# Optimization experiments

Measured on AMD Instinct MI355X. Metric: run time of the kernel, lower is better.

## Reference

```python
import jax, jax.numpy as jnp
import numpy as np

B, S, IN, E, H, FF, L = 8, 1024, 128, 512, 8, 2048, 4
HD = E // H
EPS = 1e-5


def make_pe(seq_len, d_model):
    position = np.arange(seq_len, dtype=np.float32)[:, None]
    div_term = np.exp(np.arange(0, d_model, 2, dtype=np.float32) * (-np.log(10000.0) / d_model))
    pe = np.zeros((seq_len, d_model), dtype=np.float32)
    pe[:, 0::2] = np.sin(position * div_term)
    pe[:, 1::2] = np.cos(position * div_term)
    return jnp.asarray(pe)


def setup_inputs() -> dict:
    key = jax.random.key(0)
    ks = jax.random.split(key, 16)
    s = 0.02
    return {
        "src": jax.random.normal(ks[0], (B, S, IN), jnp.float32),
        "distances": jax.random.uniform(ks[1], (B, S, S), jnp.float32),
        "proj_w": jax.random.normal(ks[2], (E, IN), jnp.float32) * s,
        "proj_b": jnp.zeros((E,), jnp.float32),
        "bn_g": jnp.ones((E,), jnp.float32),
        "bn_b": jnp.zeros((E,), jnp.float32),
        "in_proj_w": jax.random.normal(ks[3], (3 * E, E), jnp.float32) * s,
        "in_proj_b": jnp.zeros((3 * E,), jnp.float32),
        "dist_scale": jnp.array(1.0, jnp.float32),
        "lin1_w": jax.random.normal(ks[4], (FF, E), jnp.float32) * s,
        "lin1_b": jnp.zeros((FF,), jnp.float32),
        "lin2_w": jax.random.normal(ks[5], (E, FF), jnp.float32) * s,
        "lin2_b": jnp.zeros((E,), jnp.float32),
        "n1_g": jnp.ones((E,), jnp.float32),
        "n1_b": jnp.zeros((E,), jnp.float32),
        "n2_g": jnp.ones((E,), jnp.float32),
        "n2_b": jnp.zeros((E,), jnp.float32),
    }


def layernorm(x, g, b):
    m = jnp.mean(x, axis=-1, keepdims=True)
    v = jnp.var(x, axis=-1, keepdims=True)
    return (x - m) * jax.lax.rsqrt(v + EPS) * g + b


def reference(src, distances, proj_w, proj_b, bn_g, bn_b, in_proj_w, in_proj_b,
              dist_scale, lin1_w, lin1_b, lin2_w, lin2_b, n1_g, n1_b, n2_g, n2_b):
    # input projection
    x = jnp.einsum('bsi,ei->bse', src, proj_w) + proj_b  # [B,S,E]
    # BatchNorm1d over flattened (B*S) dim, training-mode batch stats
    xf = x.reshape(-1, E)
    mu = jnp.mean(xf, axis=0)
    var = jnp.var(xf, axis=0)
    x = ((xf - mu) * jax.lax.rsqrt(var + EPS) * bn_g + bn_b).reshape(B, S, E)
    # positional encoding
    x = x + make_pe(S, E)[None]
    # distance bias (same for every layer)
    dmax = jnp.max(distances, axis=-1, keepdims=True)
    dist_bias = jnp.exp(dist_scale * (1.0 - distances / dmax))  # [B,S,S]
    scale = 1.0 / jnp.sqrt(jnp.float32(HD))
    # num_layers iterations of the SAME (shared-parameter) layer
    for _ in range(L):
        qkv = jnp.einsum('bse,fe->bsf', x, in_proj_w) + in_proj_b  # [B,S,3E]
        q, k, v = jnp.split(qkv, 3, axis=-1)
        q = q.reshape(B, S, H, HD).transpose(0, 2, 1, 3)
        k = k.reshape(B, S, H, HD).transpose(0, 2, 1, 3)
        scores = jnp.einsum('bhqd,bhkd->bhqk', q, k) * scale  # [B,H,S,S]
        attn = jax.nn.softmax(scores, axis=-1)
        avg_w = jnp.mean(attn, axis=1)  # head-averaged weights [B,S,S]
        w = avg_w * dist_bias
        w = w / jnp.sum(w, axis=-1, keepdims=True)
        # NOTE: original bmm uses raw layer input as value (no V/out projection)
        attn_out = jnp.einsum('bqk,bke->bqe', w, x)
        x = layernorm(x + attn_out, n1_g, n1_b)
        ff = jnp.einsum('bsf,ef->bse', jax.nn.relu(jnp.einsum('bse,fe->bsf', x, lin1_w) + lin1_b), lin2_w) + lin2_b
        x = layernorm(x + ff, n2_g, n2_b)
    return x
```

## Files before the change

kernel.cpp:

```cpp
#include <hip/hip_runtime.h>
#include <hip/hip_bf16.h>
#include <math.h>

#define Bz 8
#define Sz 1024
#define INz 128
#define Ez 512
#define Hz 8
#define HDz 64
#define FFz 2048
#define Lz 4
#define Nz (Bz*Sz)
#define EPSf 1e-5f

typedef __attribute__((ext_vector_type(8))) short short8;
typedef __attribute__((ext_vector_type(4))) float floatx4;
#define MFMA16(a,b,c) __builtin_amdgcn_mfma_f32_16x16x32_bf16(a,b,c,0,0,0)

typedef __hip_bfloat16 bf16;

__device__ inline float b2f(bf16 v) { return __bfloat162float(v); }
__device__ inline bf16 f2b(float v) { return __float2bfloat16(v); }

__device__ inline void gload16(const bf16* g, bf16* lds_base)
{
  __builtin_amdgcn_global_load_lds(
      (const __attribute__((address_space(1))) void*)g,
      (__attribute__((address_space(3))) void*)lds_base,
      16, 0, 0);
}

#define FENCE() asm volatile("" ::: "memory")
#define PB() do { FENCE(); __builtin_amdgcn_s_barrier(); FENCE(); } while (0)
#define VMCNT0() asm volatile("s_waitcnt vmcnt(0)" ::: "memory")
#define VMCNT8() asm volatile("s_waitcnt vmcnt(8)" ::: "memory")

__global__ __launch_bounds__(256) void cast_f2b(const float* __restrict__ in,
    bf16* __restrict__ out, int n)
{
  int i = blockIdx.x * 256 + threadIdx.x;
  if (i < n) out[i] = f2b(in[i]);
}

__global__ __launch_bounds__(512, 1) void gemm256(
    const bf16* __restrict__ A, const bf16* __restrict__ Wm,
    const float* __restrict__ bias, bf16* __restrict__ Cb,
    int N, int K, int relu)
{
  int gx = gridDim.x, nwg = gx * gridDim.y;
  int flat = blockIdx.y * gx + blockIdx.x;
  if (!(nwg & 7)) {
    int cpx = nwg >> 3;
    flat = (flat & 7) * cpx + (flat >> 3);
  }
  int bm = (flat / gx) * 256, bn = (flat % gx) * 256;
  __shared__ __align__(16) bf16 As0[256][64], Bs0[256][64];
  __shared__ __align__(16) bf16 As1[256][64], Bs1[256][64];
  int t = threadIdx.x, wave = t >> 6, lane = t & 63;
  int wm = (wave >> 2) * 128, wn = (wave & 3) * 64;
  int fr = lane & 15, fo = lane >> 4;
  int w8 = wave * 8, lrow = lane >> 3;
  int sc8 = ((lane & 7) ^ (lrow & 7)) * 8;
  floatx4 acc[8][4];
  #pragma unroll
  for (int i = 0; i < 8; ++i)
    #pragma unroll
    for (int j = 0; j < 4; ++j) acc[i][j] = (floatx4){0.f, 0.f, 0.f, 0.f};

  #define STAGE8(DA, DB, kk) do {                                           \
    _Pragma("unroll")                                                        \
    for (int c_ = 0; c_ < 4; ++c_) {                                         \
      int row_ = c_ * 64 + w8 + lrow;                                        \
      gload16(A  + (size_t)(bm + row_) * K + (kk) + sc8, &DA[c_ * 64 + w8][0]);\
      gload16(Wm + (size_t)(bn + row_) * K + (kk) + sc8, &DB[c_ * 64 + w8][0]);\
    } } while (0)

  #define TILE(AA, BB, SA, SB, kk, DOSTAGE) do {                            \
    _Pragma("unroll")                                                        \
    for (int q_ = 0; q_ < 4; ++q_) {                                         \
      short8 a_[4][2], bf_[2][2];                                            \
      _Pragma("unroll")                                                      \
      for (int j_ = 0; j_ < 4; ++j_) {                                       \
        int row_ = wm + ((q_ >> 1) * 4 + j_) * 16 + fr;                      \
        a_[j_][0] = *(const short8*)&AA[row_][((fo) ^ (fr & 7)) * 8];        \
        a_[j_][1] = *(const short8*)&AA[row_][((4 + fo) ^ (fr & 7)) * 8];    \
      }                                                                      \
      _Pragma("unroll")                                                      \
      for (int g_ = 0; g_ < 2; ++g_) {                                       \
        int row_ = wn + ((q_ & 1) * 2 + g_) * 16 + fr;                       \
        bf_[g_][0] = *(const short8*)&BB[row_][((fo) ^ (fr & 7)) * 8];       \
        bf_[g_][1] = *(const short8*)&BB[row_][((4 + fo) ^ (fr & 7)) * 8];   \
      }                                                                      \
      if ((DOSTAGE) && q_ == 0) STAGE8(SA, SB, kk);                          \
      PB();                                                                  \
      __builtin_amdgcn_s_setprio(1);                                         \
      _Pragma("unroll")                                                      \
      for (int j_ = 0; j_ < 4; ++j_)                                         \
        _Pragma("unroll")                                                    \
        for (int g_ = 0; g_ < 2; ++g_) {                                     \
          int fi_ = (q_ >> 1) * 4 + j_, gi_ = (q_ & 1) * 2 + g_;             \
          acc[fi_][gi_] = MFMA16(a_[j_][0], bf_[g_][0], acc[fi_][gi_]);      \
          acc[fi_][gi_] = MFMA16(a_[j_][1], bf_[g_][1], acc[fi_][gi_]);      \
        }                                                                    \
      __builtin_amdgcn_s_setprio(0);                                         \
      if (q_ == 3) VMCNT0();                                                 \
      PB();                                                                  \
    } } while (0)

  int nt = K >> 6;
  STAGE8(As0, Bs0, 0);
  STAGE8(As1, Bs1, 64);
  VMCNT8();
  PB();
  TILE(As0, Bs0, As0, Bs0, 0, 0);
  for (int i = 1; i + 2 < nt; i += 2) {
    TILE(As1, Bs1, As0, Bs0, (i + 1) * 64, 1);
    TILE(As0, Bs0, As1, Bs1, (i + 2) * 64, 1);
  }
  TILE(As1, Bs1, As0, Bs0, 0, 0);
  #undef STAGE8
  #undef TILE

  #pragma unroll
  for (int f = 0; f < 8; ++f) {
    #pragma unroll
    for (int r = 0; r < 4; ++r) {
      int row = bm + wm + f * 16 + (lane >> 4) * 4 + r;
      #pragma unroll
      for (int g = 0; g < 4; ++g) {
        int col = bn + wn + g * 16 + fr;
        float v = acc[f][g][r] + (bias ? bias[col] : 0.f);
        if (relu) v = fmaxf(v, 0.f);
        Cb[(size_t)row * N + col] = f2b(v);
      }
    }
  }
}

__global__ __launch_bounds__(256) void gemm_bt(
    const bf16* __restrict__ A, const bf16* __restrict__ Wm,
    const float* __restrict__ bias, float* __restrict__ Cf,
    bf16* __restrict__ Cb, const float* __restrict__ rowscale,
    int M, int N, int K, long sA, long sW, long sC, int relu)
{
  int z = blockIdx.z;
  A  += (size_t)z * sA;
  Wm += (size_t)z * sW;
  if (rowscale) rowscale += (size_t)z * M;
  size_t cbase = (size_t)z * sC;
  int bm = blockIdx.y * 128, bn = blockIdx.x * 128;
  __shared__ __align__(16) bf16 As0[128][64], Bs0[128][64];
  __shared__ __align__(16) bf16 As1[128][64], Bs1[128][64];
  int t = threadIdx.x, wave = t >> 6, lane = t & 63;
  int wm = (wave >> 1) * 64, wn = (wave & 1) * 64;
  int fr = lane & 15, fo = lane >> 4;
  int srow = lane >> 3;
  int scol = ((lane & 7) ^ srow) * 8;
  floatx4 acc[4][4];
  #pragma unroll
  for (int i = 0; i < 4; ++i)
    #pragma unroll
    for (int j = 0; j < 4; ++j) acc[i][j] = (floatx4){0.f, 0.f, 0.f, 0.f};

  #define STAGE(Ad, Bd, kk) do {                                            \
    _Pragma("unroll")                                                        \
    for (int i_ = 0; i_ < 4; ++i_) {                                         \
      int chunk_ = wave * 4 + i_;                                            \
      int row_ = chunk_ * 8 + srow;                                          \
      gload16(A  + (size_t)(bm + row_) * K + (kk) + scol, &Ad[chunk_ * 8][0]);\
      gload16(Wm + (size_t)(bn + row_) * K + (kk) + scol, &Bd[chunk_ * 8][0]);\
    } } while (0)

  #define COMPUTE(Ad, Bd) do {                                               \
    _Pragma("unroll")                                                        \
    for (int ks_ = 0; ks_ < 2; ++ks_) {                                      \
      int sw_ = ((ks_ * 4 + fo) ^ (fr & 7)) * 8;                             \
      short8 af_[4], bf_[4];                                                 \
      _Pragma("unroll")                                                      \
      for (int rt_ = 0; rt_ < 4; ++rt_)                                      \
        af_[rt_] = *(const short8*)&Ad[wm + rt_ * 16 + fr][sw_];             \
      _Pragma("unroll")                                                      \
      for (int ct_ = 0; ct_ < 4; ++ct_)                                      \
        bf_[ct_] = *(const short8*)&Bd[wn + ct_ * 16 + fr][sw_];             \
      _Pragma("unroll")                                                      \
      for (int rt_ = 0; rt_ < 4; ++rt_)                                      \
        _Pragma("unroll")                                                    \
        for (int ct_ = 0; ct_ < 4; ++ct_)                                    \
          acc[rt_][ct_] = MFMA16(af_[rt_], bf_[ct_], acc[rt_][ct_]);         \
    } } while (0)

  STAGE(As0, Bs0, 0);
  __syncthreads();
  for (int k0 = 0; k0 < K; k0 += 128) {
    if (k0 + 64 < K) STAGE(As1, Bs1, k0 + 64);
    COMPUTE(As0, Bs0);
    __syncthreads();
    if (k0 + 64 < K) {
      if (k0 + 128 < K) STAGE(As0, Bs0, k0 + 128);
      COMPUTE(As1, Bs1);
      __syncthreads();
    }
  }
  #undef STAGE
  #undef COMPUTE

  #pragma unroll
  for (int rt = 0; rt < 4; ++rt) {
    #pragma unroll
    for (int r = 0; r < 4; ++r) {
      int row = bm + wm + rt * 16 + (lane >> 4) * 4 + r;
      float rs = rowscale ? (1.f / rowscale[row]) : 1.f;
      #pragma unroll
      for (int ct = 0; ct < 4; ++ct) {
        int col = bn + wn + ct * 16 + fr;
        float v = acc[rt][ct][r] + (bias ? bias[col] : 0.f);
        if (relu) v = fmaxf(v, 0.f);
        v *= rs;
        if (Cf) Cf[cbase + (size_t)row * N + col] = v;
        if (Cb) Cb[cbase + (size_t)row * N + col] = f2b(v);
      }
    }
  }
}

__global__ __launch_bounds__(256) void bn_stats(const float* __restrict__ x, float* __restrict__ st)
{
  int c = blockIdx.x;
  float s = 0.f, q = 0.f;
  for (int r = threadIdx.x; r < Nz; r += 256) {
    float v = x[(size_t)r * Ez + c];
    s += v; q += v * v;
  }
  for (int o = 32; o; o >>= 1) { s += __shfl_down(s, o); q += __shfl_down(q, o); }
  __shared__ float shs[4], shq[4];
  int w = threadIdx.x >> 6;
  if ((threadIdx.x & 63) == 0) { shs[w] = s; shq[w] = q; }
  __syncthreads();
  if (threadIdx.x == 0) {
    s = shs[0] + shs[1] + shs[2] + shs[3];
    q = shq[0] + shq[1] + shq[2] + shq[3];
    float mu = s / (float)Nz;
    float var = q / (float)Nz - mu * mu;
    st[c] = mu;
    st[Ez + c] = rsqrtf(var + EPSf);
  }
}

__global__ __launch_bounds__(256) void bn_apply_pe(const float* __restrict__ x0,
    const float* __restrict__ st, const float* __restrict__ g,
    const float* __restrict__ b, float* __restrict__ x, bf16* __restrict__ xb)
{
  int idx = blockIdx.x * 256 + threadIdx.x;
  int c = idx & (Ez - 1);
  int r = idx >> 9;
  int s = r & (Sz - 1);
  float dt = expf((float)(c & ~1) * (-9.210340371976184f / (float)Ez));
  float ang = (float)s * dt;
  float pe = (c & 1) ? cosf(ang) : sinf(ang);
  float mu = st[c], rs = st[Ez + c];
  float v = (x0[idx] - mu) * rs * g[c] + b[c] + pe;
  x[idx] = v;
  xb[idx] = f2b(v);
}

__global__ __launch_bounds__(256) void dist_bias_k(const float* __restrict__ dist,
    const float* __restrict__ dsc, bf16* __restrict__ db)
{
  size_t base = (size_t)blockIdx.x * Sz;
  float m = -1e30f;
  for (int j = threadIdx.x; j < Sz; j += 256) m = fmaxf(m, dist[base + j]);
  for (int o = 32; o; o >>= 1) m = fmaxf(m, __shfl_down(m, o));
  __shared__ float sh[4];
  if ((threadIdx.x & 63) == 0) sh[threadIdx.x >> 6] = m;
  __syncthreads();
  m = fmaxf(fmaxf(sh[0], sh[1]), fmaxf(sh[2], sh[3]));
  float sc = dsc[0];
  float inv = 1.f / m;
  for (int j = threadIdx.x; j < Sz; j += 256)
    db[base + j] = f2b(expf(sc * (1.f - dist[base + j] * inv)));
}

__global__ __launch_bounds__(256) void transpose_xb(const bf16* __restrict__ xb,
    bf16* __restrict__ xT)
{
  int b = blockIdx.z, e0 = blockIdx.y * 32, s0 = blockIdx.x * 32;
  __shared__ bf16 T[32][40];
  int t = threadIdx.x, row = t >> 3, c = t & 7;
  *(ushort4*)&T[row][c * 4] = *(const ushort4*)(xb + (size_t)(b * Sz + s0 + row) * Ez + e0 + c * 4);
  __syncthreads();
  ushort4 v;
  unsigned short* vp = (unsigned short*)&v;
  #pragma unroll
  for (int i = 0; i < 4; ++i) vp[i] = *(const unsigned short*)&T[c * 4 + i][row];
  *(ushort4*)(xT + ((size_t)b * Ez + e0 + row) * Sz + s0 + c * 4) = v;
}

__global__ __launch_bounds__(256) void attn_stats2(const bf16* __restrict__ qk,
    float* __restrict__ stats, float* __restrict__ den)
{
  int qt = blockIdx.x, h = blockIdx.y, b = blockIdx.z;
  int q0 = qt * 64;
  int t = threadIdx.x, wave = t >> 6, lane = t & 63;
  if (h == 0 && t < 64) den[(size_t)b * Sz + q0 + t] = 0.f;
  __shared__ bf16 Qs[64][72];
  __shared__ bf16 Ks[128][72];
  int fr = lane & 15, fo = (lane >> 4) * 8;
  #pragma unroll
  for (int i = 0; i < 2; ++i) {
    int idx = i * 256 + t, row = idx >> 3, c4 = idx & 7;
    *(float4*)&Qs[row][c4 * 8] =
      *(const float4*)(qk + (size_t)(b * Sz + q0 + row) * 1024 + h * 64 + c4 * 8);
  }
  __syncthreads();
  short8 aq0 = *(const short8*)&Qs[wave * 16 + fr][fo];
  short8 aq1 = *(const short8*)&Qs[wave * 16 + fr][32 + fo];
  float m_run[4] = {-1e30f, -1e30f, -1e30f, -1e30f};
  float z_run[4] = {0.f, 0.f, 0.f, 0.f};
  for (int k0 = 0; k0 < Sz; k0 += 128) {
    __syncthreads();
    #pragma unroll
    for (int i = 0; i < 4; ++i) {
      int idx = i * 256 + t, row = idx >> 3, c4 = idx & 7;
      *(float4*)&Ks[row][c4 * 8] =
        *(const float4*)(qk + (size_t)(b * Sz + k0 + row) * 1024 + 512 + h * 64 + c4 * 8);
    }
    __syncthreads();
    float sc[8][4];
    #pragma unroll
    for (int j = 0; j < 8; ++j) {
      floatx4 a4 = (floatx4){0.f, 0.f, 0.f, 0.f};
      short8 b0 = *(const short8*)&Ks[j * 16 + fr][fo];
      short8 b1 = *(const short8*)&Ks[j * 16 + fr][32 + fo];
      a4 = MFMA16(aq0, b0, a4);
      a4 = MFMA16(aq1, b1, a4);
      #pragma unroll
      for (int r = 0; r < 4; ++r) sc[j][r] = a4[r] * 0.125f;
    }
    #pragma unroll
    for (int r = 0; r < 4; ++r) {
      float vm = sc[0][r];
      #pragma unroll
      for (int j = 1; j < 8; ++j) vm = fmaxf(vm, sc[j][r]);
      #pragma unroll
      for (int o = 1; o < 16; o <<= 1) vm = fmaxf(vm, __shfl_xor(vm, o, 16));
      float mn = fmaxf(m_run[r], vm);
      float zb = 0.f;
      #pragma unroll
      for (int j = 0; j < 8; ++j) zb += __expf(sc[j][r] - mn);
      #pragma unroll
      for (int o = 1; o < 16; o <<= 1) zb += __shfl_xor(zb, o, 16);
      z_run[r] = z_run[r] * __expf(m_run[r] - mn) + zb;
      m_run[r] = mn;
    }
  }
  if (fr == 0) {
    int qb = q0 + wave * 16 + (lane >> 4) * 4;
    #pragma unroll
    for (int r = 0; r < 4; ++r) {
      size_t o = ((size_t)(b * Hz + h) * Sz + qb + r) * 2;
      stats[o] = m_run[r];
      stats[o + 1] = z_run[r];
    }
  }
}

__global__ __launch_bounds__(256) void scores_bias(const bf16* __restrict__ qk,
    const bf16* __restrict__ db, const float* __restrict__ stats,
    bf16* __restrict__ aw, float* __restrict__ den)
{
  int kt = blockIdx.x, qt = blockIdx.y, b = blockIdx.z;
  int q0 = qt * 128, k0 = kt * 128;
  __shared__ __align__(16) bf16 Qs0[128][64], Ks0[128][64];
  __shared__ __align__(16) bf16 Qs1[128][64], Ks1[128][64];
  __shared__ float mS[128][9];
  __shared__ float ziS[128][9];
  int t = threadIdx.x, wave = t >> 6, lane = t & 63;
  int fr = lane & 15, fo = lane >> 4;
  int wm = (wave >> 1) * 64, wn = (wave & 1) * 64;
  int srow = lane >> 3;
  int scol = ((lane & 7) ^ srow) * 8;
  int sw0 = ((fo) ^ (fr & 7)) * 8, sw1 = ((4 + fo) ^ (fr & 7)) * 8;

  #pragma unroll
  for (int i = 0; i < 4; ++i) {
    int lin = i * 256 + t, h = lin >> 7, q = lin & 127;
    const float* sp = stats + ((size_t)(b * Hz + h) * Sz + q0 + q) * 2;
    mS[q][h] = sp[0];
    ziS[q][h] = 1.f / sp[1];
  }

  floatx4 pac[4][4];
  #pragma unroll
  for (int i = 0; i < 4; ++i)
    #pragma unroll
    for (int j = 0; j < 4; ++j) pac[i][j] = (floatx4){0.f, 0.f, 0.f, 0.f};

  #define STAGEH(Qd, Kd, hh) do {                                            \
    _Pragma("unroll")                                                        \
    for (int i_ = 0; i_ < 4; ++i_) {                                         \
      int chunk_ = wave * 4 + i_, row_ = chunk_ * 8 + srow;                  \
      gload16(qk + (size_t)(b * Sz + q0 + row_) * 1024 + (hh) * 64 + scol,   \
              &Qd[chunk_ * 8][0]);                                           \
      gload16(qk + (size_t)(b * Sz + k0 + row_) * 1024 + 512 + (hh) * 64 + scol,\
              &Kd[chunk_ * 8][0]);                                           \
    } } while (0)

  #define HCOMP(Qd, Kd, hh) do {                                             \
    short8 bfv0[4], bfv1[4];                                                 \
    _Pragma("unroll")                                                        \
    for (int ct = 0; ct < 4; ++ct) {                                         \
      bfv0[ct] = *(const short8*)&Kd[wn + ct * 16 + fr][sw0];                \
      bfv1[ct] = *(const short8*)&Kd[wn + ct * 16 + fr][sw1];                \
    }                                                                        \
    _Pragma("unroll")                                                        \
    for (int rt = 0; rt < 4; ++rt) {                                         \
      short8 af0 = *(const short8*)&Qd[wm + rt * 16 + fr][sw0];              \
      short8 af1 = *(const short8*)&Qd[wm + rt * 16 + fr][sw1];              \
      floatx4 sc[4];                                                         \
      _Pragma("unroll")                                                      \
      for (int ct = 0; ct < 4; ++ct) {                                       \
        floatx4 z4 = (floatx4){0.f, 0.f, 0.f, 0.f};                          \
        z4 = MFMA16(af0, bfv0[ct], z4);                                      \
        sc[ct] = MFMA16(af1, bfv1[ct], z4);                                  \
      }                                                                      \
      _Pragma("unroll")                                                      \
      for (int r = 0; r < 4; ++r) {                                          \
        int qloc = wm + rt * 16 + (lane >> 4) * 4 + r;                       \
        float m = mS[qloc][hh], zi = ziS[qloc][hh];                          \
        _Pragma("unroll")                                                    \
        for (int ct = 0; ct < 4; ++ct)                                       \
          pac[rt][ct][r] += __expf(sc[ct][r] * 0.125f - m) * zi;             \
      }                                                                      \
    } } while (0)

  STAGEH(Qs0, Ks0, 0);
  __syncthreads();
  #pragma unroll 1
  for (int h = 0; h < 8; h += 2) {
    STAGEH(Qs1, Ks1, h + 1);
    HCOMP(Qs0, Ks0, h);
    __syncthreads();
    if (h + 2 < 8) STAGEH(Qs0, Ks0, h + 2);
    HCOMP(Qs1, Ks1, h + 1);
    __syncthreads();
  }
  #undef STAGEH
  #undef HCOMP

  #pragma unroll
  for (int rt = 0; rt < 4; ++rt) {
    #pragma unroll
    for (int r = 0; r < 4; ++r) {
      int qloc = wm + rt * 16 + (lane >> 4) * 4 + r;
      size_t rowoff = (size_t)(b * Sz + q0 + qloc) * Sz + k0;
      float rsum = 0.f;
      #pragma unroll
      for (int ct = 0; ct < 4; ++ct) {
        int kloc = wn + ct * 16 + fr;
        float p = pac[rt][ct][r] * 0.125f * b2f(db[rowoff + kloc]);
        aw[rowoff + kloc] = f2b(p);
        rsum += p;
      }
      #pragma unroll
      for (int o = 1; o < 16; o <<= 1) rsum += __shfl_xor(rsum, o, 16);
      if (fr == 0) atomicAdd(den + (size_t)b * Sz + q0 + qloc, rsum);
    }
  }
}

__global__ __launch_bounds__(256) void add_ln(const float* __restrict__ xin,
    const float* __restrict__ dly, const float* __restrict__ g,
    const float* __restrict__ bb, float* __restrict__ xout, bf16* __restrict__ xbout)
{
  size_t base = (size_t)blockIdx.x * Ez;
  int t = threadIdx.x;
  float2 xi = *(const float2*)(xin + base + t * 2);
  float2 dl = *(const float2*)(dly + base + t * 2);
  float a0 = xi.x + dl.x;
  float a1 = xi.y + dl.y;
  float s = a0 + a1, q = a0 * a0 + a1 * a1;
  for (int o = 32; o; o >>= 1) { s += __shfl_down(s, o); q += __shfl_down(q, o); }
  __shared__ float shs[4], shq[4];
  if ((t & 63) == 0) { shs[t >> 6] = s; shq[t >> 6] = q; }
  __syncthreads();
  s = shs[0] + shs[1] + shs[2] + shs[3];
  q = shq[0] + shq[1] + shq[2] + shq[3];
  float mu = s * (1.f / Ez);
  float var = q * (1.f / Ez) - mu * mu;
  float rs = rsqrtf(var + EPSf);
  float v0 = (a0 - mu) * rs * g[t * 2] + bb[t * 2];
  float v1 = (a1 - mu) * rs * g[t * 2 + 1] + bb[t * 2 + 1];
  float2 vo; vo.x = v0; vo.y = v1;
  *(float2*)(xout + base + t * 2) = vo;
  bf16 b0 = f2b(v0), b1 = f2b(v1);
  ushort2 pk;
  pk.x = *(unsigned short*)&b0;
  pk.y = *(unsigned short*)&b1;
  *(ushort2*)(xbout + base + t * 2) = pk;
}

extern "C" void kernel_launch(void* const* d_in, const int* in_sizes, int n_in,
                              void* d_out, int out_size, void* d_ws, size_t ws_size,
                              hipStream_t stream)
{
  const float* src        = (const float*)d_in[0];
  const float* distances  = (const float*)d_in[1];
  const float* proj_w     = (const float*)d_in[2];
  const float* proj_b     = (const float*)d_in[3];
  const float* bn_g       = (const float*)d_in[4];
  const float* bn_b       = (const float*)d_in[5];
  const float* in_proj_w  = (const float*)d_in[6];
  const float* in_proj_b  = (const float*)d_in[7];
  const float* dist_scale = (const float*)d_in[8];
  const float* lin1_w     = (const float*)d_in[9];
  const float* lin1_b     = (const float*)d_in[10];
  const float* lin2_w     = (const float*)d_in[11];
  const float* lin2_b     = (const float*)d_in[12];
  const float* n1_g       = (const float*)d_in[13];
  const float* n1_b       = (const float*)d_in[14];
  const float* n2_g       = (const float*)d_in[15];
  const float* n2_b       = (const float*)d_in[16];

  float* x = (float*)d_out;

  float* stats = (float*)d_ws;
  float* den   = stats + 131072;
  float* bnst  = den + 8192;
  float* aout  = bnst + 1024;
  float* x0    = aout;
  bf16* db_b = (bf16*)(aout + (size_t)Nz * Ez);
  bf16* Rqk  = db_b + (size_t)Bz * Sz * Sz;
  bf16* qk   = Rqk;
  bf16* aw   = Rqk + (size_t)Nz * 1024;
  bf16* ff1  = Rqk;
  bf16* xb   = Rqk + (size_t)Nz * FFz;
  bf16* xT   = xb + (size_t)Nz * Ez;
  bf16* srcb = xT + (size_t)Bz * Ez * Sz;
  bf16* wpr  = srcb + (size_t)Nz * INz;
  bf16* wqk  = wpr + Ez * INz;
  bf16* wl1  = wqk + 1024 * Ez;
  bf16* wl2  = wl1 + FFz * Ez;

  cast_f2b<<<(Nz * INz) / 256, 256, 0, stream>>>(src, srcb, Nz * INz);
  cast_f2b<<<(Ez * INz + 255) / 256, 256, 0, stream>>>(proj_w, wpr, Ez * INz);
  cast_f2b<<<(1024 * Ez) / 256, 256, 0, stream>>>(in_proj_w, wqk, 1024 * Ez);
  cast_f2b<<<(FFz * Ez) / 256, 256, 0, stream>>>(lin1_w, wl1, FFz * Ez);
  cast_f2b<<<(Ez * FFz) / 256, 256, 0, stream>>>(lin2_w, wl2, Ez * FFz);

  gemm_bt<<<dim3(Ez / 128, Nz / 128, 1), 256, 0, stream>>>(
      srcb, wpr, proj_b, x0, nullptr, nullptr, Nz, Ez, INz, 0, 0, 0, 0);
  bn_stats<<<Ez, 256, 0, stream>>>(x0, bnst);
  bn_apply_pe<<<(Nz * Ez) / 256, 256, 0, stream>>>(x0, bnst, bn_g, bn_b, x, xb);
  dist_bias_k<<<Bz * Sz, 256, 0, stream>>>(distances, dist_scale, db_b);

  for (int l = 0; l < Lz; ++l) {
    transpose_xb<<<dim3(Sz / 32, Ez / 32, Bz), 256, 0, stream>>>(xb, xT);
    gemm_bt<<<dim3(1024 / 128, Nz / 128, 1), 256, 0, stream>>>(
        xb, wqk, in_proj_b, nullptr, qk, nullptr, Nz, 1024, Ez, 0, 0, 0, 0);
    attn_stats2<<<dim3(Sz / 64, Hz, Bz), 256, 0, stream>>>(qk, stats, den);
    scores_bias<<<dim3(Sz / 128, Sz / 128, Bz), 256, 0, stream>>>(qk, db_b, stats, aw, den);
    gemm_bt<<<dim3(Ez / 128, Sz / 128, Bz), 256, 0, stream>>>(
        aw, xT, nullptr, aout, nullptr, den,
        Sz, Ez, Sz, (long)Sz * Sz, (long)Ez * Sz, (long)Sz * Ez, 0);
    add_ln<<<Nz, 256, 0, stream>>>(x, aout, n1_g, n1_b, x, xb);
    gemm256<<<dim3(FFz / 256, Nz / 256), 512, 0, stream>>>(
        xb, wl1, lin1_b, ff1, FFz, Ez, 1);
    gemm_bt<<<dim3(Ez / 128, Nz / 128, 1), 256, 0, stream>>>(
        ff1, wl2, lin2_b, aout, nullptr, nullptr, Nz, Ez, FFz, 0, 0, 0, 0);
    add_ln<<<Nz, 256, 0, stream>>>(x, aout, n2_g, n2_b, x, xb);
  }
}
```

Before: 1.127 ms.

## Split-K the PV and FF2 GEMMs in two and merge partials in add_ln

Adds split-K support to gemm_bt via per-split strides and leading dimensions. The attention-value GEMM and the second FFN GEMM run with K split in two, doubling the grid. The first split stores fp32 with bias, the second stores bf16 into dead scratch buffers, and add_ln sums both before normalizing. This aims to fill the GPU better, at the cost of extra partial-result traffic and a bf16 rounding of one partial sum.

```diff
diff --git a/kernel.cpp b/kernel.cpp
--- a/kernel.cpp
+++ b/kernel.cpp
@@ -21,6 +21,7 @@
 
 __device__ inline float b2f(bf16 v) { return __bfloat162float(v); }
 __device__ inline bf16 f2b(float v) { return __float2bfloat16(v); }
+__device__ inline float us2f(unsigned short u) { return __uint_as_float((unsigned)u << 16); }
 
 __device__ inline void gload16(const bf16* g, bf16* lds_base)
 {
@@ -141,13 +142,17 @@
     const bf16* __restrict__ A, const bf16* __restrict__ Wm,
     const float* __restrict__ bias, float* __restrict__ Cf,
     bf16* __restrict__ Cb, const float* __restrict__ rowscale,
-    int M, int N, int K, long sA, long sW, long sC, int relu)
+    int M, int N, int K, int lda, int ldw,
+    long sA, long sW, long sC, long sAk, long sWk, int nkc, int relu)
 {
   int z = blockIdx.z;
-  A  += (size_t)z * sA;
-  Wm += (size_t)z * sW;
-  if (rowscale) rowscale += (size_t)z * M;
-  size_t cbase = (size_t)z * sC;
+  int bq = z / nkc, kc = z - bq * nkc;
+  A  += (size_t)bq * sA + (size_t)kc * sAk;
+  Wm += (size_t)bq * sW + (size_t)kc * sWk;
+  if (rowscale) rowscale += (size_t)bq * M;
+  size_t cbase = (size_t)bq * sC;
+  const float* biasp = (kc == 0) ? bias : nullptr;
+  int wrCf = (kc == 0), wrCb = (kc == nkc - 1);
   int bm = blockIdx.y * 128, bn = blockIdx.x * 128;
   __shared__ __align__(16) bf16 As0[128][64], Bs0[128][64];
   __shared__ __align__(16) bf16 As1[128][64], Bs1[128][64];
@@ -167,8 +172,8 @@
     for (int i_ = 0; i_ < 4; ++i_) {                                         \
       int chunk_ = wave * 4 + i_;                                            \
       int row_ = chunk_ * 8 + srow;                                          \
-      gload16(A  + (size_t)(bm + row_) * K + (kk) + scol, &Ad[chunk_ * 8][0]);\
-      gload16(Wm + (size_t)(bn + row_) * K + (kk) + scol, &Bd[chunk_ * 8][0]);\
+      gload16(A  + (size_t)(bm + row_) * lda + (kk) + scol, &Ad[chunk_ * 8][0]);\
+      gload16(Wm + (size_t)(bn + row_) * ldw + (kk) + scol, &Bd[chunk_ * 8][0]);\
     } } while (0)
 
   #define COMPUTE(Ad, Bd) do {                                               \
@@ -213,11 +218,11 @@
       #pragma unroll
       for (int ct = 0; ct < 4; ++ct) {
         int col = bn + wn + ct * 16 + fr;
-        float v = acc[rt][ct][r] + (bias ? bias[col] : 0.f);
+        float v = acc[rt][ct][r] + (biasp ? biasp[col] : 0.f);
         if (relu) v = fmaxf(v, 0.f);
         v *= rs;
-        if (Cf) Cf[cbase + (size_t)row * N + col] = v;
-        if (Cb) Cb[cbase + (size_t)row * N + col] = f2b(v);
+        if (Cf && wrCf) Cf[cbase + (size_t)row * N + col] = v;
+        if (Cb && wrCb) Cb[cbase + (size_t)row * N + col] = f2b(v);
       }
     }
   }
@@ -469,8 +474,9 @@
 }
 
 __global__ __launch_bounds__(256) void add_ln(const float* __restrict__ xin,
-    const float* __restrict__ dly, const float* __restrict__ g,
-    const float* __restrict__ bb, float* __restrict__ xout, bf16* __restrict__ xbout)
+    const float* __restrict__ dly, const bf16* __restrict__ dly2,
+    const float* __restrict__ g, const float* __restrict__ bb,
+    float* __restrict__ xout, bf16* __restrict__ xbout)
 {
   size_t base = (size_t)blockIdx.x * Ez;
   int t = threadIdx.x;
@@ -478,6 +484,11 @@
   float2 dl = *(const float2*)(dly + base + t * 2);
   float a0 = xi.x + dl.x;
   float a1 = xi.y + dl.y;
+  if (dly2) {
+    ushort2 u = *(const ushort2*)(dly2 + base + t * 2);
+    a0 += us2f(u.x);
+    a1 += us2f(u.y);
+  }
   float s = a0 + a1, q = a0 * a0 + a1 * a1;
   for (int o = 32; o; o >>= 1) { s += __shfl_down(s, o); q += __shfl_down(q, o); }
   __shared__ float shs[4], shq[4];
@@ -540,6 +551,8 @@
   bf16* wqk  = wpr + Ez * INz;
   bf16* wl1  = wqk + 1024 * Ez;
   bf16* wl2  = wl1 + FFz * Ez;
+  bf16* pvs2 = qk;
+  bf16* ffs2 = xT;
 
   cast_f2b<<<(Nz * INz) / 256, 256, 0, stream>>>(src, srcb, Nz * INz);
   cast_f2b<<<(Ez * INz + 255) / 256, 256, 0, stream>>>(proj_w, wpr, Ez * INz);
@@ -548,7 +561,8 @@
   cast_f2b<<<(Ez * FFz) / 256, 256, 0, stream>>>(lin2_w, wl2, Ez * FFz);
 
   gemm_bt<<<dim3(Ez / 128, Nz / 128, 1), 256, 0, stream>>>(
-      srcb, wpr, proj_b, x0, nullptr, nullptr, Nz, Ez, INz, 0, 0, 0, 0);
+      srcb, wpr, proj_b, x0, nullptr, nullptr,
+      Nz, Ez, INz, INz, INz, 0, 0, 0, 0, 0, 1, 0);
   bn_stats<<<Ez, 256, 0, stream>>>(x0, bnst);
   bn_apply_pe<<<(Nz * Ez) / 256, 256, 0, stream>>>(x0, bnst, bn_g, bn_b, x, xb);
   dist_bias_k<<<Bz * Sz, 256, 0, stream>>>(distances, dist_scale, db_b);
@@ -556,17 +570,20 @@
   for (int l = 0; l < Lz; ++l) {
     transpose_xb<<<dim3(Sz / 32, Ez / 32, Bz), 256, 0, stream>>>(xb, xT);
     gemm_bt<<<dim3(1024 / 128, Nz / 128, 1), 256, 0, stream>>>(
-        xb, wqk, in_proj_b, nullptr, qk, nullptr, Nz, 1024, Ez, 0, 0, 0, 0);
+        xb, wqk, in_proj_b, nullptr, qk, nullptr,
+        Nz, 1024, Ez, Ez, Ez, 0, 0, 0, 0, 0, 1, 0);
     attn_stats2<<<dim3(Sz / 64, Hz, Bz), 256, 0, stream>>>(qk, stats, den);
     scores_bias<<<dim3(Sz / 128, Sz / 128, Bz), 256, 0, stream>>>(qk, db_b, stats, aw, den);
-    gemm_bt<<<dim3(Ez / 128, Sz / 128, Bz), 256, 0, stream>>>(
-        aw, xT, nullptr, aout, nullptr, den,
-        Sz, Ez, Sz, (long)Sz * Sz, (long)Ez * Sz, (long)Sz * Ez, 0);
-    add_ln<<<Nz, 256, 0, stream>>>(x, aout, n1_g, n1_b, x, xb);
+    gemm_bt<<<dim3(Ez / 128, Sz / 128, Bz * 2), 256, 0, stream>>>(
+        aw, xT, nullptr, aout, pvs2, den,
+        Sz, Ez, 512, Sz, Sz,
+        (long)Sz * Sz, (long)Ez * Sz, (long)Sz * Ez, 512, 512, 2, 0);
+    add_ln<<<Nz, 256, 0, stream>>>(x, aout, pvs2, n1_g, n1_b, x, xb);
     gemm256<<<dim3(FFz / 256, Nz / 256), 512, 0, stream>>>(
         xb, wl1, lin1_b, ff1, FFz, Ez, 1);
-    gemm_bt<<<dim3(Ez / 128, Nz / 128, 1), 256, 0, stream>>>(
-        ff1, wl2, lin2_b, aout, nullptr, nullptr, Nz, Ez, FFz, 0, 0, 0, 0);
-    add_ln<<<Nz, 256, 0, stream>>>(x, aout, n2_g, n2_b, x, xb);
-  }
-}
+    gemm_bt<<<dim3(Ez / 128, Nz / 128, 2), 256, 0, stream>>>(
+        ff1, wl2, lin2_b, aout, ffs2, nullptr,
+        Nz, Ez, 1024, FFz, FFz, 0, 0, 0, 1024, 1024, 2, 0);
+    add_ln<<<Nz, 256, 0, stream>>>(x, aout, ffs2, n2_g, n2_b, x, xb);
+  }
+}
```

Result: no change. 1.147 ms (+1.7%).
